# Performance work log

Measured on AMD Instinct MI355X. Metric: run time of the kernel, lower is better.

Reference implementation:

```python
import jax, jax.numpy as jnp
import numpy as np
from jax import lax

B, C, H, W = 16, 256, 32, 32
DH = 32
HEADS = C // DH          # 8
WSZ = 4                  # window size
K = 4                    # top-k windows
MR = 4                   # mlp_ratio
NWIN = (H // WSZ) * (W // WSZ)  # 64
WS = WSZ * WSZ                  # 16 tokens per window
EPS = 1e-5


def setup_inputs() -> dict:
    key = jax.random.key(0)
    ks = jax.random.split(key, 8)
    w = lambda i, shape: jax.random.normal(ks[i], shape, jnp.float32) * 0.02
    d = {
        'x': jax.random.normal(ks[0], (B, C, H, W), jnp.float32),
        'bn0_g': jax.random.uniform(ks[1], (C,), jnp.float32, 0.5, 1.5),
        'bn0_b': jnp.zeros((C,), jnp.float32),
        'bn0_m': jnp.zeros((C,), jnp.float32),
        'bn0_v': jnp.ones((C,), jnp.float32),
        'w_qkv': w(2, (3 * C, C)),
        'w_merge': w(3, (C, C)),
        'b_merge': jnp.zeros((C,), jnp.float32),
        'w1': w(4, (MR * C, C)),
        'bn1_g': jax.random.uniform(ks[5], (MR * C,), jnp.float32, 0.5, 1.5),
        'bn1_b': jnp.zeros((MR * C,), jnp.float32),
        'bn1_m': jnp.zeros((MR * C,), jnp.float32),
        'bn1_v': jnp.ones((MR * C,), jnp.float32),
        'dw': w(6, (MR * C, 1, 3, 3)),
        'bn2_g': jax.random.uniform(ks[7], (MR * C,), jnp.float32, 0.5, 1.5),
        'bn2_b': jnp.zeros((MR * C,), jnp.float32),
        'bn2_m': jnp.zeros((MR * C,), jnp.float32),
        'bn2_v': jnp.ones((MR * C,), jnp.float32),
        'w2': w(0, (C, MR * C)),
        'bn3_g': jax.random.uniform(ks[1], (C,), jnp.float32, 0.5, 1.5),
        'bn3_b': jnp.zeros((C,), jnp.float32),
        'bn3_m': jnp.zeros((C,), jnp.float32),
        'bn3_v': jnp.ones((C,), jnp.float32),
    }
    return d


def _bn(x, g, b, m, v):
    # eval-mode BatchNorm2d on NCHW
    s = (g / jnp.sqrt(v + EPS))
    return (x - m[None, :, None, None]) * s[None, :, None, None] + b[None, :, None, None]


def _win(t):
    # [B, C, H, W] -> [B, HEADS, NWIN, WS, DH]
    nh, nw = H // WSZ, W // WSZ
    t = t.reshape(B, HEADS, DH, nh, WSZ, nw, WSZ)
    return t.transpose(0, 1, 3, 5, 4, 6, 2).reshape(B, HEADS, NWIN, WS, DH)


def _unwin(t):
    # [B, HEADS, NWIN, WS, DH] -> [B, C, H, W]
    nh, nw = H // WSZ, W // WSZ
    t = t.reshape(B, HEADS, nh, nw, WSZ, WSZ, DH)
    return t.transpose(0, 1, 6, 2, 4, 3, 5).reshape(B, C, H, W)


def _forward(x, bn0_g, bn0_b, bn0_m, bn0_v, w_qkv, w_merge, b_merge,
             w1, bn1_g, bn1_b, bn1_m, bn1_v, dw, bn2_g, bn2_b, bn2_m, bn2_v,
             w2, bn3_g, bn3_b, bn3_m, bn3_v):
    # qkv projection: BN -> GELU -> 1x1 conv (no bias)
    h = jax.nn.gelu(_bn(x, bn0_g, bn0_b, bn0_m, bn0_v), approximate=False)
    qkv = jnp.einsum('oc,bchw->bohw', w_qkv, h)
    q, k, v = jnp.split(qkv, 3, axis=1)

    qw, kw, vw = _win(q), _win(k), _win(v)  # [B,H,NWIN,WS,DH]
    scale = 1.0 / jnp.sqrt(jnp.float32(DH))

    # window-level descriptors -> window-window affinity -> top-k selection
    wsc = jnp.einsum('bhid,bhjd->bhij', qw.mean(3), kw.mean(3)) * scale
    idx = lax.top_k(wsc, K)[1]  # [B,H,NWIN,K]

    # gather top-k kv windows per query window (irregular access)
    gather = jax.vmap(jax.vmap(lambda t, ix: t[ix]))  # over B, HEADS
    kk = gather(kw, idx).reshape(B, HEADS, NWIN, K * WS, DH)
    vv = gather(vw, idx).reshape(B, HEADS, NWIN, K * WS, DH)

    attn = jax.nn.softmax(jnp.einsum('bhnqd,bhnkd->bhnqk', qw, kk) * scale, axis=-1)
    msg = jnp.einsum('bhnqk,bhnkd->bhnqd', attn, vv)
    msg = _unwin(msg)

    # merge (1x1 conv with bias) + residual
    x = x + jnp.einsum('oc,bchw->bohw', w_merge, msg) + b_merge[None, :, None, None]

    # MB mlp: 1x1 expand -> BN -> GELU -> depthwise 3x3 -> BN -> GELU -> 1x1 -> BN
    h = jnp.einsum('oc,bchw->bohw', w1, x)
    h = jax.nn.gelu(_bn(h, bn1_g, bn1_b, bn1_m, bn1_v), approximate=False)
    h = lax.conv_general_dilated(h, dw, (1, 1), 'SAME',
                                 feature_group_count=MR * C,
                                 dimension_numbers=('NCHW', 'OIHW', 'NCHW'))
    h = jax.nn.gelu(_bn(h, bn2_g, bn2_b, bn2_m, bn2_v), approximate=False)
    h = jnp.einsum('oc,bchw->bohw', w2, h)
    h = _bn(h, bn3_g, bn3_b, bn3_m, bn3_v)
    return x + h


def reference(x, bn0_g, bn0_b, bn0_m, bn0_v, w_qkv, w_merge, b_merge,
              w1, bn1_g, bn1_b, bn1_m, bn1_v, dw, bn2_g, bn2_b, bn2_m, bn2_v,
              w2, bn3_g, bn3_b, bn3_m, bn3_v):
    return _forward(x, bn0_g, bn0_b, bn0_m, bn0_v, w_qkv, w_merge, b_merge,
                    w1, bn1_g, bn1_b, bn1_m, bn1_v, dw, bn2_g, bn2_b, bn2_m, bn2_v,
                    w2, bn3_g, bn3_b, bn3_m, bn3_v)
```

## Files before the change

kernel.cpp:

```cpp
#include <hip/hip_runtime.h>
#include <hip/hip_bf16.h>

#define EPSV 1e-5f

typedef short bf16x8 __attribute__((ext_vector_type(8)));
typedef float f32x4 __attribute__((ext_vector_type(4)));

__device__ __forceinline__ float gelu_f(float x) {
    return 0.5f * x * (1.0f + erff(x * 0.70710678118654752f));
}
__device__ __forceinline__ float b2f(unsigned short u) {
    union { float f; unsigned i; } c; c.i = ((unsigned)u) << 16; return c.f;
}
__device__ __forceinline__ unsigned short f2b(float f) {
    __hip_bfloat16 h = __float2bfloat16(f);
    return *reinterpret_cast<unsigned short*>(&h);
}
__device__ __forceinline__ float lo16f(unsigned v) {
    union { float f; unsigned i; } c; c.i = v << 16; return c.f;
}
__device__ __forceinline__ float hi16f(unsigned v) {
    union { float f; unsigned i; } c; c.i = v & 0xffff0000u; return c.f;
}
__device__ __forceinline__ void gload16(const unsigned short* g, unsigned short* l) {
    __builtin_amdgcn_global_load_lds(
        (const __attribute__((address_space(1))) void*)g,
        (__attribute__((address_space(3))) void*)l, 16, 0, 0);
}

__global__ __launch_bounds__(256) void wcvt_k(const float* __restrict__ w,
                                              unsigned short* __restrict__ o, int n4) {
    int i = blockIdx.x * 256 + threadIdx.x;
    if (i >= n4) return;
    float4 v = ((const float4*)w)[i];
    ushort4 u = make_ushort4(f2b(v.x), f2b(v.y), f2b(v.z), f2b(v.w));
    ((ushort4*)o)[i] = u;
}

__global__ __launch_bounds__(256) void wprep_k(const float* __restrict__ wdw,
    const float* __restrict__ g, const float* __restrict__ bt,
    const float* __restrict__ mu, const float* __restrict__ va,
    float* __restrict__ wt, float* __restrict__ scf, float* __restrict__ shf) {
    int ch = blockIdx.x * 256 + threadIdx.x;
    #pragma unroll
    for (int tap = 0; tap < 9; ++tap)
        wt[tap * 1024 + ch] = wdw[ch * 9 + tap];
    float s = g[ch] * rsqrtf(va[ch] + EPSV);
    scf[ch] = s;
    shf[ch] = bt[ch] - mu[ch] * s;
}

__global__ __launch_bounds__(256) void bn0tr_k(const float* __restrict__ x,
    const float* __restrict__ g, const float* __restrict__ bt,
    const float* __restrict__ mu, const float* __restrict__ va,
    unsigned short* __restrict__ h0b, float* __restrict__ xt) {
    __shared__ float tile[64][65];
    int hw0 = blockIdx.x * 64, c0 = blockIdx.y * 64, b = blockIdx.z;
    int t = threadIdx.x;
    int cl = t >> 6, hl = t & 63;
    #pragma unroll
    for (int r = 0; r < 16; ++r)
        tile[r * 4 + cl][hl] = x[((size_t)(b * 256 + c0 + r * 4 + cl)) * 1024 + hw0 + hl];
    __syncthreads();
    int c = c0 + (t & 63);
    float s = g[c] * rsqrtf(va[c] + EPSV);
    float m_ = mu[c], be = bt[c];
    #pragma unroll
    for (int r = 0; r < 16; ++r) {
        int hl2 = r * 4 + (t >> 6);
        float v = tile[t & 63][hl2];
        size_t o = ((size_t)(b * 1024 + hw0 + hl2)) * 256 + c;
        xt[o] = v;
        h0b[o] = f2b(gelu_f((v - m_) * s + be));
    }
}

__global__ __launch_bounds__(256) void hm_k(const float* __restrict__ xt,
    const float* __restrict__ g, const float* __restrict__ bt,
    const float* __restrict__ mu, const float* __restrict__ va,
    float* __restrict__ hm) {
    int blk = blockIdx.x;
    int b = blk >> 6, win = blk & 63;
    int c = threadIdx.x;
    int base = (win >> 3) * 128 + (win & 7) * 4;
    float s = g[c] * rsqrtf(va[c] + EPSV);
    float m_ = mu[c], be = bt[c];
    float acc = 0.f;
    #pragma unroll
    for (int ty = 0; ty < 4; ++ty)
        #pragma unroll
        for (int tx = 0; tx < 4; ++tx) {
            float v = xt[((size_t)(b * 1024 + base + ty * 32 + tx)) * 256 + c];
            acc += gelu_f((v - m_) * s + be);
        }
    hm[(size_t)blk * 256 + c] = acc * (1.f / 16.f);
}

template <int MODE>
__global__ __launch_bounds__(256) void mgemm(
    const unsigned short* __restrict__ A, const unsigned short* __restrict__ X,
    unsigned short* __restrict__ outb, float* __restrict__ outf,
    const float* __restrict__ res,
    const float* __restrict__ p0, const float* __restrict__ p1,
    const float* __restrict__ p2, const float* __restrict__ p3,
    int M, int Kd) {
    __shared__ __align__(16) unsigned short As[4096];
    __shared__ __align__(16) unsigned short Bs[4096];
    const int t = threadIdx.x;
    const int wid = t >> 6, lane = t & 63;
    const int n0 = blockIdx.x * 128, m0 = blockIdx.y * 128, b = blockIdx.z;
    const unsigned short* Ab = A + (size_t)m0 * Kd;
    const unsigned short* Xb = X + ((size_t)b * 1024 + n0) * Kd;

    const int srow = lane >> 2;
    const int skb  = (lane & 3) * 8;
    const int wr = wid >> 1, wc = wid & 1;
    const int lr = lane & 15;
    const int lk = (lane >> 4) * 8;

    f32x4 acc[4][4] = {};

    for (int k0 = 0; k0 < Kd; k0 += 32) {
        #pragma unroll
        for (int i = 0; i < 2; ++i) {
            int chunk = wid * 2 + i;
            int row = chunk * 16 + srow;
            gload16(Ab + (size_t)row * Kd + k0 + skb, &As[chunk * 512]);
            gload16(Xb + (size_t)row * Kd + k0 + skb, &Bs[chunk * 512]);
        }
        __syncthreads();
        bf16x8 af[4], bfv[4];
        #pragma unroll
        for (int mi = 0; mi < 4; ++mi)
            af[mi] = *(const bf16x8*)&As[(wr * 64 + mi * 16 + lr) * 32 + lk];
        #pragma unroll
        for (int ni = 0; ni < 4; ++ni)
            bfv[ni] = *(const bf16x8*)&Bs[(wc * 64 + ni * 16 + lr) * 32 + lk];
        #pragma unroll
        for (int mi = 0; mi < 4; ++mi)
            #pragma unroll
            for (int ni = 0; ni < 4; ++ni)
                acc[mi][ni] = __builtin_amdgcn_mfma_f32_16x16x32_bf16(
                    af[mi], bfv[ni], acc[mi][ni], 0, 0, 0);
        __syncthreads();
    }

    const int crow = (lane >> 4) * 4;
    #pragma unroll
    for (int ni = 0; ni < 4; ++ni) {
        const int n = n0 + wc * 64 + ni * 16 + lr;
        #pragma unroll
        for (int mi = 0; mi < 4; ++mi) {
            const int m = m0 + wr * 64 + mi * 16 + crow;
            f32x4 v = acc[mi][ni];
            size_t o = ((size_t)b * 1024 + n) * (size_t)M + m;
            if (MODE == 0) {
                *(ushort4*)(outb + o) = make_ushort4(f2b(v[0]), f2b(v[1]), f2b(v[2]), f2b(v[3]));
            } else if (MODE == 1) {
                float4 r = *(const float4*)(res + o);
                float4 bi = *(const float4*)(p0 + m);
                float w0 = v[0] + r.x + bi.x, w1 = v[1] + r.y + bi.y;
                float w2 = v[2] + r.z + bi.z, w3 = v[3] + r.w + bi.w;
                *(float4*)(outf + o) = make_float4(w0, w1, w2, w3);
                *(ushort4*)(outb + o) = make_ushort4(f2b(w0), f2b(w1), f2b(w2), f2b(w3));
            } else if (MODE == 2) {
                float4 gg = *(const float4*)(p0 + m);
                float4 be = *(const float4*)(p1 + m);
                float4 mm = *(const float4*)(p2 + m);
                float4 vv = *(const float4*)(p3 + m);
                float h0 = gelu_f((v[0] - mm.x) * (gg.x * rsqrtf(vv.x + EPSV)) + be.x);
                float h1 = gelu_f((v[1] - mm.y) * (gg.y * rsqrtf(vv.y + EPSV)) + be.y);
                float h2 = gelu_f((v[2] - mm.z) * (gg.z * rsqrtf(vv.z + EPSV)) + be.z);
                float h3 = gelu_f((v[3] - mm.w) * (gg.w * rsqrtf(vv.w + EPSV)) + be.w);
                *(ushort4*)(outb + o) = make_ushort4(f2b(h0), f2b(h1), f2b(h2), f2b(h3));
            } else {
                float4 gg = *(const float4*)(p0 + m);
                float4 be = *(const float4*)(p1 + m);
                float4 mm = *(const float4*)(p2 + m);
                float4 vv = *(const float4*)(p3 + m);
                float4 r = *(const float4*)(res + o);
                float y0 = (v[0] - mm.x) * (gg.x * rsqrtf(vv.x + EPSV)) + be.x + r.x;
                float y1 = (v[1] - mm.y) * (gg.y * rsqrtf(vv.y + EPSV)) + be.y + r.y;
                float y2 = (v[2] - mm.z) * (gg.z * rsqrtf(vv.z + EPSV)) + be.z + r.z;
                float y3 = (v[3] - mm.w) * (gg.w * rsqrtf(vv.w + EPSV)) + be.w + r.w;
                *(float4*)(outf + o) = make_float4(y0, y1, y2, y3);
            }
        }
    }
}

__global__ __launch_bounds__(256) void desc2_k(const float* __restrict__ hm,
                                               const float* __restrict__ w_qkv,
                                               float* __restrict__ qkd) {
    __shared__ float As[16][64];
    __shared__ float Bs[16][64];
    float acc[4][4] = {{0.f}};
    const int t = threadIdx.x;
    const int tn = t & 15, tm = t >> 4;
    const int n0 = blockIdx.x * 64;
    const int m0 = blockIdx.y * 64;
    for (int k0 = 0; k0 < 256; k0 += 16) {
        {
            int r  = t >> 2;
            int k4 = (t & 3) << 2;
            float4 a4 = *(const float4*)(w_qkv + (size_t)(m0 + r) * 256 + k0 + k4);
            As[k4 + 0][r] = a4.x; As[k4 + 1][r] = a4.y;
            As[k4 + 2][r] = a4.z; As[k4 + 3][r] = a4.w;
            float4 b4 = *(const float4*)(hm + (size_t)(n0 + r) * 256 + k0 + k4);
            Bs[k4 + 0][r] = b4.x; Bs[k4 + 1][r] = b4.y;
            Bs[k4 + 2][r] = b4.z; Bs[k4 + 3][r] = b4.w;
        }
        __syncthreads();
        #pragma unroll
        for (int kk = 0; kk < 16; ++kk) {
            float4 av = *(const float4*)&As[kk][tm << 2];
            float4 bv = *(const float4*)&Bs[kk][tn << 2];
            float a0[4] = {av.x, av.y, av.z, av.w};
            float b0[4] = {bv.x, bv.y, bv.z, bv.w};
            #pragma unroll
            for (int i = 0; i < 4; ++i)
                #pragma unroll
                for (int j = 0; j < 4; ++j)
                    acc[i][j] += a0[i] * b0[j];
        }
        __syncthreads();
    }
    #pragma unroll
    for (int j = 0; j < 4; ++j) {
        int row = n0 + (tn << 2) + j;
        float4 v = make_float4(acc[0][j], acc[1][j], acc[2][j], acc[3][j]);
        *(float4*)(qkd + (size_t)row * 512 + m0 + (tm << 2)) = v;
    }
}

__global__ __launch_bounds__(256) void aff_k(const float* __restrict__ qkd,
                                             int* __restrict__ idx_out) {
    int bh = blockIdx.x;
    int b = bh >> 3, h = bh & 7;
    __shared__ float qdl[64][33];
    __shared__ float kdl[64][33];
    __shared__ float wsc[64][65];
    int t = threadIdx.x;
    for (int e = t; e < 2048; e += 256) {
        int wn = e >> 5, d = e & 31;
        size_t src = ((size_t)(b * 64 + wn)) * 512 + h * 32 + d;
        qdl[wn][d] = qkd[src];
        kdl[wn][d] = qkd[src + 256];
    }
    __syncthreads();
    {
        int i = t >> 2, j0 = (t & 3) * 16;
        float s[16];
        #pragma unroll
        for (int j = 0; j < 16; ++j) s[j] = 0.f;
        #pragma unroll
        for (int d = 0; d < 32; ++d) {
            float qv = qdl[i][d];
            #pragma unroll
            for (int j = 0; j < 16; ++j) s[j] += qv * kdl[j0 + j][d];
        }
        #pragma unroll
        for (int j = 0; j < 16; ++j) wsc[i][j0 + j] = s[j];
    }
    __syncthreads();
    if (t < 64) {
        float bv[4] = {-1e30f, -1e30f, -1e30f, -1e30f};
        int   bi[4] = {0, 0, 0, 0};
        for (int j = 0; j < 64; ++j) {
            float v = wsc[t][j];
            if (v > bv[3]) {
                int p = 3;
                while (p > 0 && v > bv[p - 1]) {
                    bv[p] = bv[p - 1]; bi[p] = bi[p - 1]; --p;
                }
                bv[p] = v; bi[p] = j;
            }
        }
        int* o = idx_out + (bh * 64 + t) * 4;
        o[0] = bi[0]; o[1] = bi[1]; o[2] = bi[2]; o[3] = bi[3];
    }
}

__global__ __launch_bounds__(256) void attn_k(const unsigned short* __restrict__ qkv,
                                              const int* __restrict__ idx,
                                              unsigned short* __restrict__ msg) {
    __shared__ __align__(16) unsigned short qs[4][16][40];
    __shared__ __align__(16) unsigned short ks[4][64][40];
    __shared__ __align__(16) unsigned short vt[4][32][72];
    __shared__ __align__(16) unsigned short ps[4][16][72];
    const int t = threadIdx.x;
    const int wid = t >> 6, lane = t & 63;
    const int g = blockIdx.x * 4 + wid;
    const int win = g & 63;
    const int bh = g >> 6;
    const int b = bh >> 3, h = bh & 7;
    const int qb = (win >> 3) * 128 + (win & 7) * 4;
    const int* widx = idx + (bh * 64 + win) * 4;

    for (int e = lane; e < 128; e += 64) {
        int tok = e >> 3, d4 = (e & 7) * 4;
        int hw = qb + (tok >> 2) * 32 + (tok & 3);
        uint2 u = *(const uint2*)&qkv[((size_t)(b * 1024 + hw)) * 768 + h * 32 + d4];
        *(uint2*)&qs[wid][tok][d4] = u;
    }
    for (int e = lane; e < 512; e += 64) {
        int key = e >> 3, d4 = (e & 7) * 4;
        int wsel = widx[key >> 4];
        int tok = key & 15;
        int hw = (wsel >> 3) * 128 + (wsel & 7) * 4 + (tok >> 2) * 32 + (tok & 3);
        size_t base = ((size_t)(b * 1024 + hw)) * 768 + h * 32 + d4;
        uint2 uk = *(const uint2*)&qkv[base + 256];
        uint2 uv = *(const uint2*)&qkv[base + 512];
        *(uint2*)&ks[wid][key][d4] = uk;
        vt[wid][d4 + 0][key] = (unsigned short)(uv.x & 0xffffu);
        vt[wid][d4 + 1][key] = (unsigned short)(uv.x >> 16);
        vt[wid][d4 + 2][key] = (unsigned short)(uv.y & 0xffffu);
        vt[wid][d4 + 3][key] = (unsigned short)(uv.y >> 16);
    }
    __syncthreads();

    const int lr = lane & 15;
    const int lk8 = (lane >> 4) * 8;
    const float scale = 0.17677669529663688f;
    f32x4 zero = {0.f, 0.f, 0.f, 0.f};

    bf16x8 qA = *(const bf16x8*)&qs[wid][lr][lk8];
    f32x4 sa[4];
    #pragma unroll
    for (int kt = 0; kt < 4; ++kt) {
        bf16x8 kB = *(const bf16x8*)&ks[wid][kt * 16 + lr][lk8];
        sa[kt] = __builtin_amdgcn_mfma_f32_16x16x32_bf16(qA, kB, zero, 0, 0, 0);
    }
    #pragma unroll
    for (int i = 0; i < 4; ++i) {
        float s0 = sa[0][i] * scale, s1 = sa[1][i] * scale;
        float s2 = sa[2][i] * scale, s3 = sa[3][i] * scale;
        float mx = fmaxf(fmaxf(s0, s1), fmaxf(s2, s3));
        #pragma unroll
        for (int m = 1; m < 16; m <<= 1) mx = fmaxf(mx, __shfl_xor(mx, m));
        float e0 = expf(s0 - mx), e1 = expf(s1 - mx);
        float e2 = expf(s2 - mx), e3 = expf(s3 - mx);
        float sm = e0 + e1 + e2 + e3;
        #pragma unroll
        for (int m = 1; m < 16; m <<= 1) sm += __shfl_xor(sm, m);
        float inv = 1.0f / sm;
        int row = (lane >> 4) * 4 + i;
        ps[wid][row][ 0 + lr] = f2b(e0 * inv);
        ps[wid][row][16 + lr] = f2b(e1 * inv);
        ps[wid][row][32 + lr] = f2b(e2 * inv);
        ps[wid][row][48 + lr] = f2b(e3 * inv);
    }
    __syncthreads();
    f32x4 oa[2] = {zero, zero};
    #pragma unroll
    for (int kh = 0; kh < 2; ++kh) {
        bf16x8 pA = *(const bf16x8*)&ps[wid][lr][kh * 32 + lk8];
        #pragma unroll
        for (int nt = 0; nt < 2; ++nt) {
            bf16x8 vB = *(const bf16x8*)&vt[wid][nt * 16 + lr][kh * 32 + lk8];
            oa[nt] = __builtin_amdgcn_mfma_f32_16x16x32_bf16(pA, vB, oa[nt], 0, 0, 0);
        }
    }
    #pragma unroll
    for (int nt = 0; nt < 2; ++nt) {
        int d = nt * 16 + lr;
        #pragma unroll
        for (int i = 0; i < 4; ++i) {
            int tok = (lane >> 4) * 4 + i;
            int hw = qb + (tok >> 2) * 32 + (tok & 3);
            msg[((size_t)(b * 1024 + hw)) * 256 + h * 32 + d] = f2b(oa[nt][i]);
        }
    }
}

__global__ __launch_bounds__(256) void dw_k(const unsigned short* __restrict__ h1,
    const float* __restrict__ wt, const float* __restrict__ scf,
    const float* __restrict__ shf, unsigned short* __restrict__ h2) {
    int t = threadIdx.x;
    int c8 = t & 127;
    int pl = t >> 7;
    int blk = blockIdx.x;
    int b = blk >> 7;
    int rem = blk & 127;
    int y = rem >> 2;
    int x0 = (rem & 3) * 8;
    int ch0 = c8 * 8;

    float w[9][8];
    #pragma unroll
    for (int tap = 0; tap < 9; ++tap) {
        float4 a = *(const float4*)(wt + tap * 1024 + ch0);
        float4 bq = *(const float4*)(wt + tap * 1024 + ch0 + 4);
        w[tap][0] = a.x; w[tap][1] = a.y; w[tap][2] = a.z; w[tap][3] = a.w;
        w[tap][4] = bq.x; w[tap][5] = bq.y; w[tap][6] = bq.z; w[tap][7] = bq.w;
    }
    float sc[8], sh[8];
    {
        float4 a = *(const float4*)(scf + ch0);
        float4 bq = *(const float4*)(scf + ch0 + 4);
        sc[0]=a.x; sc[1]=a.y; sc[2]=a.z; sc[3]=a.w; sc[4]=bq.x; sc[5]=bq.y; sc[6]=bq.z; sc[7]=bq.w;
        float4 c = *(const float4*)(shf + ch0);
        float4 dq = *(const float4*)(shf + ch0 + 4);
        sh[0]=c.x; sh[1]=c.y; sh[2]=c.z; sh[3]=c.w; sh[4]=dq.x; sh[5]=dq.y; sh[6]=dq.z; sh[7]=dq.w;
    }

    const unsigned short* base = h1 + (size_t)b * 1048576;
    unsigned short* ob = h2 + (size_t)b * 1048576;

    #pragma unroll
    for (int j = 0; j < 4; ++j) {
        int x = x0 + pl + 2 * j;
        float acc[8] = {0.f,0.f,0.f,0.f,0.f,0.f,0.f,0.f};
        #pragma unroll
        for (int dy = -1; dy <= 1; ++dy) {
            int yy = y + dy;
            if (yy < 0 || yy > 31) continue;
            #pragma unroll
            for (int dx = -1; dx <= 1; ++dx) {
                int xx = x + dx;
                if (xx < 0 || xx > 31) continue;
                uint4 u = *(const uint4*)(base + (size_t)(yy * 32 + xx) * 1024 + ch0);
                int tap = (dy + 1) * 3 + (dx + 1);
                acc[0] += lo16f(u.x) * w[tap][0];
                acc[1] += hi16f(u.x) * w[tap][1];
                acc[2] += lo16f(u.y) * w[tap][2];
                acc[3] += hi16f(u.y) * w[tap][3];
                acc[4] += lo16f(u.z) * w[tap][4];
                acc[5] += hi16f(u.z) * w[tap][5];
                acc[6] += lo16f(u.w) * w[tap][6];
                acc[7] += hi16f(u.w) * w[tap][7];
            }
        }
        unsigned short r[8];
        #pragma unroll
        for (int c = 0; c < 8; ++c)
            r[c] = f2b(gelu_f(acc[c] * sc[c] + sh[c]));
        uint4 o;
        o.x = (unsigned)r[0] | ((unsigned)r[1] << 16);
        o.y = (unsigned)r[2] | ((unsigned)r[3] << 16);
        o.z = (unsigned)r[4] | ((unsigned)r[5] << 16);
        o.w = (unsigned)r[6] | ((unsigned)r[7] << 16);
        *(uint4*)(ob + (size_t)(y * 32 + x) * 1024 + ch0) = o;
    }
}

__global__ __launch_bounds__(256) void trout_k(const float* __restrict__ y,
                                               float* __restrict__ out) {
    __shared__ float tile[64][65];
    int hw0 = blockIdx.x * 64, c0 = blockIdx.y * 64, b = blockIdx.z;
    int t = threadIdx.x;
    #pragma unroll
    for (int r = 0; r < 16; ++r) {
        int hl = r * 4 + (t >> 6);
        tile[t & 63][hl] = y[((size_t)(b * 1024 + hw0 + hl)) * 256 + c0 + (t & 63)];
    }
    __syncthreads();
    #pragma unroll
    for (int r = 0; r < 16; ++r) {
        int cl = r * 4 + (t >> 6);
        out[((size_t)(b * 256 + c0 + cl)) * 1024 + hw0 + (t & 63)] = tile[cl][t & 63];
    }
}

extern "C" void kernel_launch(void* const* d_in, const int* in_sizes, int n_in,
                              void* d_out, int out_size, void* d_ws, size_t ws_size,
                              hipStream_t stream) {
    const float* x      = (const float*)d_in[0];
    const float* bn0_g  = (const float*)d_in[1];
    const float* bn0_b  = (const float*)d_in[2];
    const float* bn0_m  = (const float*)d_in[3];
    const float* bn0_v  = (const float*)d_in[4];
    const float* w_qkv  = (const float*)d_in[5];
    const float* w_merge= (const float*)d_in[6];
    const float* b_merge= (const float*)d_in[7];
    const float* w1     = (const float*)d_in[8];
    const float* bn1_g  = (const float*)d_in[9];
    const float* bn1_b  = (const float*)d_in[10];
    const float* bn1_m  = (const float*)d_in[11];
    const float* bn1_v  = (const float*)d_in[12];
    const float* dw     = (const float*)d_in[13];
    const float* bn2_g  = (const float*)d_in[14];
    const float* bn2_b  = (const float*)d_in[15];
    const float* bn2_m  = (const float*)d_in[16];
    const float* bn2_v  = (const float*)d_in[17];
    const float* w2     = (const float*)d_in[18];
    const float* bn3_g  = (const float*)d_in[19];
    const float* bn3_b  = (const float*)d_in[20];
    const float* bn3_m  = (const float*)d_in[21];
    const float* bn3_v  = (const float*)d_in[22];
    float* out = (float*)d_out;

    char* w = (char*)d_ws;
    unsigned short* h0b   = (unsigned short*)(w);
    unsigned short* qkvb  = (unsigned short*)(w + 8388608);
    unsigned short* msgb  = (unsigned short*)(w + 33554432);
    unsigned short* xrb   = (unsigned short*)(w + 41943040);
    unsigned short* h1b   = (unsigned short*)(w + 50331648);
    unsigned short* h2b   = (unsigned short*)(w + 83886080);
    float*  xt    = (float*)(w + 117440512);
    float*  xrf   = (float*)(w + 134217728);
    float*  yf    = (float*)(w + 150994944);
    float*  hm    = (float*)(w + 167772160);
    unsigned short* wqkvb = (unsigned short*)(w + 168820736);
    unsigned short* wmrgb = (unsigned short*)(w + 169213952);
    unsigned short* w1b   = (unsigned short*)(w + 169345024);
    unsigned short* w2b   = (unsigned short*)(w + 169869312);
    int*    idx   = (int*)(w + 170393600);
    float*  wtbuf = (float*)(w + 170524672);
    float*  scbuf = (float*)(w + 170561536);
    float*  shbuf = (float*)(w + 170565632);
    float*  qkdbuf= (float*)(w + 170569728);

    wcvt_k<<<192, 256, 0, stream>>>(w_qkv, wqkvb, 49152);
    wcvt_k<<<64,  256, 0, stream>>>(w_merge, wmrgb, 16384);
    wcvt_k<<<256, 256, 0, stream>>>(w1, w1b, 65536);
    wcvt_k<<<256, 256, 0, stream>>>(w2, w2b, 65536);
    wprep_k<<<4, 256, 0, stream>>>(dw, bn2_g, bn2_b, bn2_m, bn2_v, wtbuf, scbuf, shbuf);

    bn0tr_k<<<dim3(16, 4, 16), 256, 0, stream>>>(x, bn0_g, bn0_b, bn0_m, bn0_v, h0b, xt);
    hm_k<<<1024, 256, 0, stream>>>(xt, bn0_g, bn0_b, bn0_m, bn0_v, hm);
    mgemm<0><<<dim3(8, 6, 16), 256, 0, stream>>>(wqkvb, h0b, qkvb, nullptr,
        nullptr, nullptr, nullptr, nullptr, nullptr, 768, 256);
    desc2_k<<<dim3(16, 8), 256, 0, stream>>>(hm, w_qkv, qkdbuf);
    aff_k<<<128, 256, 0, stream>>>(qkdbuf, idx);
    attn_k<<<2048, 256, 0, stream>>>(qkvb, idx, msgb);
    mgemm<1><<<dim3(8, 2, 16), 256, 0, stream>>>(wmrgb, msgb, xrb, xrf,
        xt, b_merge, nullptr, nullptr, nullptr, 256, 256);
    mgemm<2><<<dim3(8, 8, 16), 256, 0, stream>>>(w1b, xrb, h1b, nullptr,
        nullptr, bn1_g, bn1_b, bn1_m, bn1_v, 1024, 256);
    dw_k<<<2048, 256, 0, stream>>>(h1b, wtbuf, scbuf, shbuf, h2b);
    mgemm<3><<<dim3(8, 2, 16), 256, 0, stream>>>(w2b, h2b, nullptr, yf,
        xrf, bn3_g, bn3_b, bn3_m, bn3_v, 256, 1024);
    trout_k<<<dim3(16, 4, 16), 256, 0, stream>>>(yf, out);
}
```

Baseline: 345.2 us.

## Fuse output transpose into final GEMM, merge weight casts, load Q directly

Result: faster. 329.2 us (-4.6%).

```diff
diff --git a/kernel.cpp b/kernel.cpp
--- a/kernel.cpp
+++ b/kernel.cpp
@@ -28,13 +28,19 @@
         (__attribute__((address_space(3))) void*)l, 16, 0, 0);
 }
 
-__global__ __launch_bounds__(256) void wcvt_k(const float* __restrict__ w,
-                                              unsigned short* __restrict__ o, int n4) {
+__global__ __launch_bounds__(256) void wcvt4_k(
+    const float* __restrict__ wqkv, const float* __restrict__ wm,
+    const float* __restrict__ w1, const float* __restrict__ w2,
+    unsigned short* __restrict__ oq, unsigned short* __restrict__ om,
+    unsigned short* __restrict__ o1, unsigned short* __restrict__ o2) {
     int i = blockIdx.x * 256 + threadIdx.x;
-    if (i >= n4) return;
-    float4 v = ((const float4*)w)[i];
-    ushort4 u = make_ushort4(f2b(v.x), f2b(v.y), f2b(v.z), f2b(v.w));
-    ((ushort4*)o)[i] = u;
+    const float* src; unsigned short* dst; int off;
+    if (i < 49152)       { src = wqkv; dst = oq; off = i; }
+    else if (i < 65536)  { src = wm;   dst = om; off = i - 49152; }
+    else if (i < 131072) { src = w1;   dst = o1; off = i - 65536; }
+    else                 { src = w2;   dst = o2; off = i - 131072; }
+    float4 v = ((const float4*)src)[off];
+    ((ushort4*)dst)[off] = make_ushort4(f2b(v.x), f2b(v.y), f2b(v.z), f2b(v.w));
 }
 
 __global__ __launch_bounds__(256) void wprep_k(const float* __restrict__ wdw,
@@ -183,7 +189,11 @@
                 float y1 = (v[1] - mm.y) * (gg.y * rsqrtf(vv.y + EPSV)) + be.y + r.y;
                 float y2 = (v[2] - mm.z) * (gg.z * rsqrtf(vv.z + EPSV)) + be.z + r.z;
                 float y3 = (v[3] - mm.w) * (gg.w * rsqrtf(vv.w + EPSV)) + be.w + r.w;
-                *(float4*)(outf + o) = make_float4(y0, y1, y2, y3);
+                size_t ob = ((size_t)b * 256 + m) * 1024 + n;
+                outf[ob]          = y0;
+                outf[ob + 1024]   = y1;
+                outf[ob + 2048]   = y2;
+                outf[ob + 3072]   = y3;
             }
         }
     }
@@ -284,7 +294,6 @@
 __global__ __launch_bounds__(256) void attn_k(const unsigned short* __restrict__ qkv,
                                               const int* __restrict__ idx,
                                               unsigned short* __restrict__ msg) {
-    __shared__ __align__(16) unsigned short qs[4][16][40];
     __shared__ __align__(16) unsigned short ks[4][64][40];
     __shared__ __align__(16) unsigned short vt[4][32][72];
     __shared__ __align__(16) unsigned short ps[4][16][72];
@@ -297,12 +306,6 @@
     const int qb = (win >> 3) * 128 + (win & 7) * 4;
     const int* widx = idx + (bh * 64 + win) * 4;
 
-    for (int e = lane; e < 128; e += 64) {
-        int tok = e >> 3, d4 = (e & 7) * 4;
-        int hw = qb + (tok >> 2) * 32 + (tok & 3);
-        uint2 u = *(const uint2*)&qkv[((size_t)(b * 1024 + hw)) * 768 + h * 32 + d4];
-        *(uint2*)&qs[wid][tok][d4] = u;
-    }
     for (int e = lane; e < 512; e += 64) {
         int key = e >> 3, d4 = (e & 7) * 4;
         int wsel = widx[key >> 4];
@@ -317,14 +320,16 @@
         vt[wid][d4 + 2][key] = (unsigned short)(uv.y & 0xffffu);
         vt[wid][d4 + 3][key] = (unsigned short)(uv.y >> 16);
     }
-    __syncthreads();
 
     const int lr = lane & 15;
     const int lk8 = (lane >> 4) * 8;
     const float scale = 0.17677669529663688f;
     f32x4 zero = {0.f, 0.f, 0.f, 0.f};
 
-    bf16x8 qA = *(const bf16x8*)&qs[wid][lr][lk8];
+    int qhw = qb + (lr >> 2) * 32 + (lr & 3);
+    bf16x8 qA = *(const bf16x8*)&qkv[((size_t)(b * 1024 + qhw)) * 768 + h * 32 + lk8];
+    __syncthreads();
+
     f32x4 sa[4];
     #pragma unroll
     for (int kt = 0; kt < 4; ++kt) {
@@ -441,24 +446,6 @@
         o.z = (unsigned)r[4] | ((unsigned)r[5] << 16);
         o.w = (unsigned)r[6] | ((unsigned)r[7] << 16);
         *(uint4*)(ob + (size_t)(y * 32 + x) * 1024 + ch0) = o;
-    }
-}
-
-__global__ __launch_bounds__(256) void trout_k(const float* __restrict__ y,
-                                               float* __restrict__ out) {
-    __shared__ float tile[64][65];
-    int hw0 = blockIdx.x * 64, c0 = blockIdx.y * 64, b = blockIdx.z;
-    int t = threadIdx.x;
-    #pragma unroll
-    for (int r = 0; r < 16; ++r) {
-        int hl = r * 4 + (t >> 6);
-        tile[t & 63][hl] = y[((size_t)(b * 1024 + hw0 + hl)) * 256 + c0 + (t & 63)];
-    }
-    __syncthreads();
-    #pragma unroll
-    for (int r = 0; r < 16; ++r) {
-        int cl = r * 4 + (t >> 6);
-        out[((size_t)(b * 256 + c0 + cl)) * 1024 + hw0 + (t & 63)] = tile[cl][t & 63];
     }
 }
 
@@ -499,7 +486,6 @@
     unsigned short* h2b   = (unsigned short*)(w + 83886080);
     float*  xt    = (float*)(w + 117440512);
     float*  xrf   = (float*)(w + 134217728);
-    float*  yf    = (float*)(w + 150994944);
     float*  hm    = (float*)(w + 167772160);
     unsigned short* wqkvb = (unsigned short*)(w + 168820736);
     unsigned short* wmrgb = (unsigned short*)(w + 169213952);
@@ -511,10 +497,7 @@
     float*  shbuf = (float*)(w + 170565632);
     float*  qkdbuf= (float*)(w + 170569728);
 
-    wcvt_k<<<192, 256, 0, stream>>>(w_qkv, wqkvb, 49152);
-    wcvt_k<<<64,  256, 0, stream>>>(w_merge, wmrgb, 16384);
-    wcvt_k<<<256, 256, 0, stream>>>(w1, w1b, 65536);
-    wcvt_k<<<256, 256, 0, stream>>>(w2, w2b, 65536);
+    wcvt4_k<<<768, 256, 0, stream>>>(w_qkv, w_merge, w1, w2, wqkvb, wmrgb, w1b, w2b);
     wprep_k<<<4, 256, 0, stream>>>(dw, bn2_g, bn2_b, bn2_m, bn2_v, wtbuf, scbuf, shbuf);
 
     bn0tr_k<<<dim3(16, 4, 16), 256, 0, stream>>>(x, bn0_g, bn0_b, bn0_m, bn0_v, h0b, xt);
@@ -529,7 +512,6 @@
     mgemm<2><<<dim3(8, 8, 16), 256, 0, stream>>>(w1b, xrb, h1b, nullptr,
         nullptr, bn1_g, bn1_b, bn1_m, bn1_v, 1024, 256);
     dw_k<<<2048, 256, 0, stream>>>(h1b, wtbuf, scbuf, shbuf, h2b);
-    mgemm<3><<<dim3(8, 2, 16), 256, 0, stream>>>(w2b, h2b, nullptr, yf,
+    mgemm<3><<<dim3(8, 2, 16), 256, 0, stream>>>(w2b, h2b, nullptr, out,
         xrf, bn3_g, bn3_b, bn3_m, bn3_v, 256, 1024);
-    trout_k<<<dim3(16, 4, 16), 256, 0, stream>>>(yf, out);
-}
+}
```
